# Optimization experiments

Hardware: AMD Instinct MI355X
Metric: run time of the kernel (lower is better)

## Reference

```python
import jax, jax.numpy as jnp
import numpy as np

D_MODEL = 1024
NUM_HEADS = 16
DEPTH = D_MODEL // NUM_HEADS
B, S = 2, 2048


def setup_inputs() -> dict:
    key = jax.random.key(0)
    ks = jax.random.split(key, 11)
    sc = 1.0 / np.sqrt(D_MODEL)
    inp = {
        "q": jax.random.normal(ks[0], (B, S, D_MODEL), jnp.float32),
        "k": jax.random.normal(ks[1], (B, S, D_MODEL), jnp.float32),
        "v": jax.random.normal(ks[2], (B, S, D_MODEL), jnp.float32),
        # 1 = masked (upper triangle), broadcastable to [B,H,S,S]
        "mask": jnp.triu(jnp.ones((S, S), jnp.float32), k=1)[None, None],
        "wq": jax.random.normal(ks[3], (D_MODEL, D_MODEL), jnp.float32) * sc,
        "bq": jnp.zeros((D_MODEL,), jnp.float32),
        "wk": jax.random.normal(ks[4], (D_MODEL, D_MODEL), jnp.float32) * sc,
        "bk": jnp.zeros((D_MODEL,), jnp.float32),
        "wv": jax.random.normal(ks[5], (D_MODEL, D_MODEL), jnp.float32) * sc,
        "bv": jnp.zeros((D_MODEL,), jnp.float32),
        "wo": jax.random.normal(ks[6], (D_MODEL, D_MODEL), jnp.float32) * sc,
        "bo": jnp.zeros((D_MODEL,), jnp.float32),
    }
    return inp


def _split_heads(x):
    b, s, _ = x.shape
    return x.reshape(b, s, NUM_HEADS, DEPTH).transpose(0, 2, 1, 3)  # [B,H,S,D]


def reference(q, k, v, mask, wq, bq, wk, bk, wv, bv, wo, bo):
    qh = _split_heads(q @ wq + bq)
    kh = _split_heads(k @ wk + bk)
    vh = _split_heads(v @ wv + bv)
    logits = jnp.einsum("bhqd,bhkd->bhqk", qh, kh) / jnp.sqrt(
        jnp.asarray(DEPTH, qh.dtype))
    logits = logits + mask * (-1e9)
    attn = jax.nn.softmax(logits, axis=-1)  # [B,H,S,S]
    ctx = jnp.einsum("bhqk,bhkd->bhqd", attn, vh)
    concat = ctx.transpose(0, 2, 1, 3).reshape(q.shape[0], -1, D_MODEL)
    out = concat @ wo + bo
    return out, attn
```

## Files before the change

### kernel.cpp

```cpp
#include <hip/hip_runtime.h>
#include <cstdint>
#include <cstddef>

#define BATCH   2
#define SEQ     2048
#define DMODEL  1024
#define NHEADS  16
#define DHEAD   64
#define TOKENS  (BATCH*SEQ)

typedef __bf16 bf16_t;
typedef bf16_t bf16x8 __attribute__((ext_vector_type(8)));
typedef bf16_t bf16x4 __attribute__((ext_vector_type(4)));
typedef float  f32x4  __attribute__((ext_vector_type(4)));

__device__ __forceinline__ f32x4 mfma16(bf16x8 a, bf16x8 b, f32x4 c) {
    return __builtin_amdgcn_mfma_f32_16x16x32_bf16(a, b, c, 0, 0, 0);
}

__global__ __launch_bounds__(256) void conv_w(
    const float* __restrict__ W, bf16_t* __restrict__ Wt)
{
    __shared__ bf16_t tl[64][65];
    const int t  = threadIdx.x;
    const int kb = blockIdx.y * 64;
    const int nb = blockIdx.x * 64;
    const int r  = t >> 2;
    const int cs = (t & 3) * 16;

    const float* src = W + (size_t)(kb + r)*DMODEL + nb + cs;
    #pragma unroll
    for (int j = 0; j < 4; ++j) {
        float4 u = ((const float4*)src)[j];
        tl[r][cs + j*4 + 0] = (bf16_t)u.x;
        tl[r][cs + j*4 + 1] = (bf16_t)u.y;
        tl[r][cs + j*4 + 2] = (bf16_t)u.z;
        tl[r][cs + j*4 + 3] = (bf16_t)u.w;
    }
    __syncthreads();
    bf16_t* dst = Wt + (size_t)(nb + r)*DMODEL + kb + cs;
    #pragma unroll
    for (int h = 0; h < 2; ++h) {
        bf16x8 o;
        #pragma unroll
        for (int j = 0; j < 8; ++j) o[j] = tl[cs + h*8 + j][r];
        *(bf16x8*)(dst + h*8) = o;
    }
}

template<int IN_BF16, int MODE>
__global__ __launch_bounds__(256, 2) void proj_gemm(
    const void* __restrict__ xin, const bf16_t* __restrict__ Wt,
    const float* __restrict__ bias, void* __restrict__ out)
{
    __shared__ __align__(16) bf16_t Xl[128*72];
    __shared__ __align__(16) bf16_t Wl[64*72];

    const int t    = threadIdx.x;
    const int w    = t >> 6;
    const int lane = t & 63;
    const int quad = lane >> 4;
    const int l16  = lane & 15;
    const int m0   = blockIdx.y * 128;
    const int n0   = blockIdx.x * 64;

    f32x4 acc[2][4] = {};

    for (int kt = 0; kt < DMODEL/64; ++kt) {
        __syncthreads();
        #pragma unroll
        for (int it = 0; it < 4; ++it) {
            int s   = t + it*256;
            int row = s >> 3, seg = s & 7;
            if (IN_BF16) {
                const bf16_t* xb = (const bf16_t*)xin + (size_t)(m0+row)*DMODEL + kt*64 + seg*8;
                *(bf16x8*)&Xl[row*72 + seg*8] = *(const bf16x8*)xb;
            } else {
                const float* xf = (const float*)xin + (size_t)(m0+row)*DMODEL + kt*64 + seg*8;
                float4 u0 = *(const float4*)xf;
                float4 u1 = *(const float4*)(xf + 4);
                bf16x8 vv;
                vv[0]=(bf16_t)u0.x; vv[1]=(bf16_t)u0.y; vv[2]=(bf16_t)u0.z; vv[3]=(bf16_t)u0.w;
                vv[4]=(bf16_t)u1.x; vv[5]=(bf16_t)u1.y; vv[6]=(bf16_t)u1.z; vv[7]=(bf16_t)u1.w;
                *(bf16x8*)&Xl[row*72 + seg*8] = vv;
            }
        }
        #pragma unroll
        for (int it = 0; it < 2; ++it) {
            int s = t + it*256;
            int n = s >> 3, seg = s & 7;
            *(bf16x8*)&Wl[n*72 + seg*8] =
                *(const bf16x8*)(Wt + (size_t)(n0+n)*DMODEL + kt*64 + seg*8);
        }
        __syncthreads();

        #pragma unroll
        for (int kk = 0; kk < 2; ++kk) {
            bf16x8 a0 = *(const bf16x8*)&Xl[(w*32      + l16)*72 + kk*32 + quad*8];
            bf16x8 a1 = *(const bf16x8*)&Xl[(w*32 + 16 + l16)*72 + kk*32 + quad*8];
            #pragma unroll
            for (int c = 0; c < 4; ++c) {
                bf16x8 b = *(const bf16x8*)&Wl[(c*16 + l16)*72 + kk*32 + quad*8];
                acc[0][c] = mfma16(a0, b, acc[0][c]);
                acc[1][c] = mfma16(a1, b, acc[1][c]);
            }
        }
    }

    #pragma unroll
    for (int r = 0; r < 2; ++r) {
        #pragma unroll
        for (int c = 0; c < 4; ++c) {
            int n = n0 + c*16 + l16;
            float bv = bias[n];
            #pragma unroll
            for (int reg = 0; reg < 4; ++reg) {
                int gm = m0 + w*32 + r*16 + quad*4 + reg;
                float val = acc[r][c][reg] + bv;
                if (MODE == 2) {
                    ((float*)out)[(size_t)gm*DMODEL + n] = val;
                } else {
                    int b = gm >> 11, sTok = gm & (SEQ-1);
                    int h = n >> 6,  d    = n & (DHEAD-1);
                    if (MODE == 0)
                        ((bf16_t*)out)[(((size_t)(b*NHEADS + h))*SEQ + sTok)*DHEAD + d] = (bf16_t)val;
                    else
                        ((bf16_t*)out)[(((size_t)(b*NHEADS + h))*DHEAD + d)*SEQ + sTok] = (bf16_t)val;
                }
            }
        }
    }
}

__global__ __launch_bounds__(256, 2) void attn_kernel(
    const bf16_t* __restrict__ Qh, const bf16_t* __restrict__ Kh,
    const bf16_t* __restrict__ Vt, float* __restrict__ attn,
    bf16_t* __restrict__ ctx)
{
    __shared__ __align__(16) bf16_t Ql[64*72];
    __shared__ __align__(16) bf16_t Kl[64*72];
    __shared__ __align__(16) bf16_t Vl[64*72];
    __shared__ __align__(16) bf16_t Pl[4][16*72];

    const int t    = threadIdx.x;
    const int w    = t >> 6;
    const int lane = t & 63;
    const int quad = lane >> 4;
    const int l16  = lane & 15;
    const int bh   = blockIdx.y;
    const int q0   = blockIdx.x * 64;

    const bf16_t* Qp = Qh + (size_t)bh * SEQ * DHEAD;
    const bf16_t* Kp = Kh + (size_t)bh * SEQ * DHEAD;
    const bf16_t* Vp = Vt + (size_t)bh * DHEAD * SEQ;
    float* attp = attn + (size_t)bh * SEQ * SEQ;

    #pragma unroll
    for (int it = 0; it < 2; ++it) {
        int s = t + it*256;
        int row = s >> 3, seg = s & 7;
        *(bf16x8*)&Ql[row*72 + seg*8] =
            *(const bf16x8*)(Qp + (size_t)(q0 + row)*DHEAD + seg*8);
    }
    __syncthreads();
    bf16x8 bq[2];
    bq[0] = *(const bf16x8*)&Ql[(w*16 + l16)*72 +      quad*8];
    bq[1] = *(const bf16x8*)&Ql[(w*16 + l16)*72 + 32 + quad*8];

    const int nkt  = q0/64 + 1;
    const int qrow = q0 + w*16 + l16;
    const float C1 = 0.18033688011112042f;

    float m2 = -1e30f, l2 = 0.f;

    for (int kt = 0; kt < nkt; ++kt) {
        __syncthreads();
        #pragma unroll
        for (int it = 0; it < 2; ++it) {
            int s = t + it*256;
            int row = s >> 3, seg = s & 7;
            *(bf16x8*)&Kl[row*72 + seg*8] =
                *(const bf16x8*)(Kp + (size_t)(kt*64 + row)*DHEAD + seg*8);
        }
        __syncthreads();

        f32x4 sf[4] = {};
        #pragma unroll
        for (int kk = 0; kk < 2; ++kk) {
            #pragma unroll
            for (int c = 0; c < 4; ++c) {
                bf16x8 ak = *(const bf16x8*)&Kl[(c*16 + l16)*72 + kk*32 + quad*8];
                sf[c] = mfma16(ak, bq[kk], sf[c]);
            }
        }
        float tm = -1e30f;
        #pragma unroll
        for (int c = 0; c < 4; ++c) {
            int colb = kt*64 + c*16 + quad*4;
            #pragma unroll
            for (int reg = 0; reg < 4; ++reg) {
                float z = sf[c][reg] * C1;
                z = (colb + reg > qrow) ? -1e30f : z;
                sf[c][reg] = z;
                tm = fmaxf(tm, z);
            }
        }
        tm = fmaxf(tm, __shfl_xor(tm, 16));
        tm = fmaxf(tm, __shfl_xor(tm, 32));
        float mnew = fmaxf(m2, tm);
        float ps = 0.f;
        #pragma unroll
        for (int c = 0; c < 4; ++c)
            #pragma unroll
            for (int reg = 0; reg < 4; ++reg)
                ps += exp2f(sf[c][reg] - mnew);
        ps += __shfl_xor(ps, 16);
        ps += __shfl_xor(ps, 32);
        l2 = l2 * exp2f(m2 - mnew) + ps;
        m2 = mnew;
    }
    const float invl = 1.0f / l2;

    f32x4 cacc[4] = {};
    bf16_t* Plw = &Pl[w][0];

    for (int kt = 0; kt < nkt; ++kt) {
        __syncthreads();
        #pragma unroll
        for (int it = 0; it < 2; ++it) {
            int s = t + it*256;
            int row = s >> 3, seg = s & 7;
            *(bf16x8*)&Kl[row*72 + seg*8] =
                *(const bf16x8*)(Kp + (size_t)(kt*64 + row)*DHEAD + seg*8);
            *(bf16x8*)&Vl[row*72 + seg*8] =
                *(const bf16x8*)(Vp + (size_t)row*SEQ + kt*64 + seg*8);
        }
        __syncthreads();

        f32x4 sf[4] = {};
        #pragma unroll
        for (int kk = 0; kk < 2; ++kk) {
            #pragma unroll
            for (int c = 0; c < 4; ++c) {
                bf16x8 ak = *(const bf16x8*)&Kl[(c*16 + l16)*72 + kk*32 + quad*8];
                sf[c] = mfma16(ak, bq[kk], sf[c]);
            }
        }
        #pragma unroll
        for (int c = 0; c < 4; ++c) {
            int colb = kt*64 + c*16 + quad*4;
            f32x4 pv;
            #pragma unroll
            for (int reg = 0; reg < 4; ++reg) {
                float z = sf[c][reg] * C1;
                float p = (colb + reg > qrow) ? 0.0f : exp2f(z - m2) * invl;
                pv[reg] = p;
            }
            __builtin_nontemporal_store(pv,
                (f32x4*)(attp + (size_t)qrow*SEQ + colb));
            bf16x4 pk;
            pk[0]=(bf16_t)pv[0]; pk[1]=(bf16_t)pv[1];
            pk[2]=(bf16_t)pv[2]; pk[3]=(bf16_t)pv[3];
            *(bf16x4*)&Plw[l16*72 + c*16 + quad*4] = pk;
        }
        #pragma unroll
        for (int kk = 0; kk < 2; ++kk) {
            bf16x8 ap = *(const bf16x8*)&Plw[l16*72 + kk*32 + quad*8];
            #pragma unroll
            for (int c = 0; c < 4; ++c) {
                bf16x8 bv = *(const bf16x8*)&Vl[(c*16 + l16)*72 + kk*32 + quad*8];
                cacc[c] = mfma16(ap, bv, cacc[c]);
            }
        }
    }

    {
        const int r = t >> 2;
        const int c4base = nkt*16 + (t & 3);
        f32x4 z = {0.f, 0.f, 0.f, 0.f};
        float* rowp = attp + (size_t)(q0 + r)*SEQ;
        for (int c4 = c4base; c4 < SEQ/4; c4 += 4)
            __builtin_nontemporal_store(z, (f32x4*)rowp + c4);
    }

    const int b = bh >> 4, h = bh & 15;
    #pragma unroll
    for (int c = 0; c < 4; ++c) {
        #pragma unroll
        for (int reg = 0; reg < 4; ++reg) {
            int gq = q0 + w*16 + quad*4 + reg;
            size_t idx = ((size_t)(b*SEQ + gq))*DMODEL + h*DHEAD + c*16 + l16;
            ctx[idx] = (bf16_t)cacc[c][reg];
        }
    }
}

extern "C" void kernel_launch(void* const* d_in, const int* in_sizes, int n_in,
                              void* d_out, int out_size, void* d_ws, size_t ws_size,
                              hipStream_t stream) {
    const float* q  = (const float*)d_in[0];
    const float* k  = (const float*)d_in[1];
    const float* v  = (const float*)d_in[2];
    const float* wq = (const float*)d_in[4];
    const float* bq = (const float*)d_in[5];
    const float* wk = (const float*)d_in[6];
    const float* bk = (const float*)d_in[7];
    const float* wv = (const float*)d_in[8];
    const float* bv = (const float*)d_in[9];
    const float* wo = (const float*)d_in[10];
    const float* bo = (const float*)d_in[11];

    float* out  = (float*)d_out;
    float* attn = out + (size_t)TOKENS * DMODEL;

    bf16_t* Qws = (bf16_t*)d_ws;
    bf16_t* Kws = Qws + (size_t)TOKENS * DMODEL;
    bf16_t* Vws = Kws + (size_t)TOKENS * DMODEL;
    bf16_t* Cws = Vws + (size_t)TOKENS * DMODEL;

    bf16_t* WtA = (bf16_t*)attn;
    bf16_t* WtB = Qws;

    dim3 blk(256);
    dim3 gconv(DMODEL/64, DMODEL/64);
    dim3 gproj(DMODEL/64, TOKENS/128);

    conv_w<<<gconv, blk, 0, stream>>>(wq, WtA);
    proj_gemm<0,0><<<gproj, blk, 0, stream>>>(q, WtA, bq, Qws);
    conv_w<<<gconv, blk, 0, stream>>>(wk, WtA);
    proj_gemm<0,0><<<gproj, blk, 0, stream>>>(k, WtA, bk, Kws);
    conv_w<<<gconv, blk, 0, stream>>>(wv, WtA);
    proj_gemm<0,1><<<gproj, blk, 0, stream>>>(v, WtA, bv, Vws);

    dim3 gattn(SEQ/64, BATCH*NHEADS);
    attn_kernel<<<gattn, blk, 0, stream>>>(Qws, Kws, Vws, attn, Cws);

    conv_w<<<gconv, blk, 0, stream>>>(wo, WtB);
    proj_gemm<1,2><<<gproj, blk, 0, stream>>>(Cws, WtB, bo, out);
}
```

Measured before the change: 937.9 us.

## Batch weight/input bf16 conversion, skip mask on off-diagonal tiles, reverse attention block order

```diff
diff --git a/kernel.cpp b/kernel.cpp
--- a/kernel.cpp
+++ b/kernel.cpp
@@ -18,7 +18,7 @@
     return __builtin_amdgcn_mfma_f32_16x16x32_bf16(a, b, c, 0, 0, 0);
 }
 
-__global__ __launch_bounds__(256) void conv_w(
+__device__ __forceinline__ void conv_w_body(
     const float* __restrict__ W, bf16_t* __restrict__ Wt)
 {
     __shared__ bf16_t tl[64][65];
@@ -48,9 +48,43 @@
     }
 }
 
-template<int IN_BF16, int MODE>
-__global__ __launch_bounds__(256, 2) void proj_gemm(
-    const void* __restrict__ xin, const bf16_t* __restrict__ Wt,
+__global__ __launch_bounds__(256) void conv_w1(
+    const float* __restrict__ W, bf16_t* __restrict__ Wt)
+{
+    conv_w_body(W, Wt);
+}
+
+__global__ __launch_bounds__(256) void conv_w3(
+    const float* __restrict__ w0, const float* __restrict__ w1,
+    const float* __restrict__ w2, bf16_t* __restrict__ t0,
+    bf16_t* __restrict__ t1, bf16_t* __restrict__ t2)
+{
+    const int z = blockIdx.z;
+    const float* W  = (z == 0) ? w0 : (z == 1) ? w1 : w2;
+    bf16_t*      Wt = (z == 0) ? t0 : (z == 1) ? t1 : t2;
+    conv_w_body(W, Wt);
+}
+
+__global__ __launch_bounds__(256) void conv_x3(
+    const float* __restrict__ x0, const float* __restrict__ x1,
+    const float* __restrict__ x2, bf16_t* __restrict__ y0,
+    bf16_t* __restrict__ y1, bf16_t* __restrict__ y2)
+{
+    const int z = blockIdx.z;
+    const float* xs = (z == 0) ? x0 : (z == 1) ? x1 : x2;
+    bf16_t*      ys = (z == 0) ? y0 : (z == 1) ? y1 : y2;
+    const size_t base = ((size_t)blockIdx.x*256 + threadIdx.x) * 8;
+    float4 u0 = ((const float4*)(xs + base))[0];
+    float4 u1 = ((const float4*)(xs + base))[1];
+    bf16x8 vv;
+    vv[0]=(bf16_t)u0.x; vv[1]=(bf16_t)u0.y; vv[2]=(bf16_t)u0.z; vv[3]=(bf16_t)u0.w;
+    vv[4]=(bf16_t)u1.x; vv[5]=(bf16_t)u1.y; vv[6]=(bf16_t)u1.z; vv[7]=(bf16_t)u1.w;
+    *(bf16x8*)(ys + base) = vv;
+}
+
+template<int MODE>
+__global__ __launch_bounds__(256, 4) void proj_gemm(
+    const bf16_t* __restrict__ xin, const bf16_t* __restrict__ Wt,
     const float* __restrict__ bias, void* __restrict__ out)
 {
     __shared__ __align__(16) bf16_t Xl[128*72];
@@ -72,18 +106,8 @@
         for (int it = 0; it < 4; ++it) {
             int s   = t + it*256;
             int row = s >> 3, seg = s & 7;
-            if (IN_BF16) {
-                const bf16_t* xb = (const bf16_t*)xin + (size_t)(m0+row)*DMODEL + kt*64 + seg*8;
-                *(bf16x8*)&Xl[row*72 + seg*8] = *(const bf16x8*)xb;
-            } else {
-                const float* xf = (const float*)xin + (size_t)(m0+row)*DMODEL + kt*64 + seg*8;
-                float4 u0 = *(const float4*)xf;
-                float4 u1 = *(const float4*)(xf + 4);
-                bf16x8 vv;
-                vv[0]=(bf16_t)u0.x; vv[1]=(bf16_t)u0.y; vv[2]=(bf16_t)u0.z; vv[3]=(bf16_t)u0.w;
-                vv[4]=(bf16_t)u1.x; vv[5]=(bf16_t)u1.y; vv[6]=(bf16_t)u1.z; vv[7]=(bf16_t)u1.w;
-                *(bf16x8*)&Xl[row*72 + seg*8] = vv;
-            }
+            *(bf16x8*)&Xl[row*72 + seg*8] =
+                *(const bf16x8*)(xin + (size_t)(m0+row)*DMODEL + kt*64 + seg*8);
         }
         #pragma unroll
         for (int it = 0; it < 2; ++it) {
@@ -132,7 +156,7 @@
     }
 }
 
-__global__ __launch_bounds__(256, 2) void attn_kernel(
+__global__ __launch_bounds__(256, 4) void attn_kernel(
     const bf16_t* __restrict__ Qh, const bf16_t* __restrict__ Kh,
     const bf16_t* __restrict__ Vt, float* __restrict__ attn,
     bf16_t* __restrict__ ctx)
@@ -148,7 +172,7 @@
     const int quad = lane >> 4;
     const int l16  = lane & 15;
     const int bh   = blockIdx.y;
-    const int q0   = blockIdx.x * 64;
+    const int q0   = (gridDim.x - 1 - blockIdx.x) * 64;
 
     const bf16_t* Qp = Qh + (size_t)bh * SEQ * DHEAD;
     const bf16_t* Kp = Kh + (size_t)bh * SEQ * DHEAD;
@@ -194,16 +218,27 @@
             }
         }
         float tm = -1e30f;
-        #pragma unroll
-        for (int c = 0; c < 4; ++c) {
-            int colb = kt*64 + c*16 + quad*4;
-            #pragma unroll
-            for (int reg = 0; reg < 4; ++reg) {
-                float z = sf[c][reg] * C1;
-                z = (colb + reg > qrow) ? -1e30f : z;
-                sf[c][reg] = z;
-                tm = fmaxf(tm, z);
-            }
+        if (kt == nkt - 1) {
+            #pragma unroll
+            for (int c = 0; c < 4; ++c) {
+                int colb = kt*64 + c*16 + quad*4;
+                #pragma unroll
+                for (int reg = 0; reg < 4; ++reg) {
+                    float z = sf[c][reg] * C1;
+                    z = (colb + reg > qrow) ? -1e30f : z;
+                    sf[c][reg] = z;
+                    tm = fmaxf(tm, z);
+                }
+            }
+        } else {
+            #pragma unroll
+            for (int c = 0; c < 4; ++c)
+                #pragma unroll
+                for (int reg = 0; reg < 4; ++reg) {
+                    float z = sf[c][reg] * C1;
+                    sf[c][reg] = z;
+                    tm = fmaxf(tm, z);
+                }
         }
         tm = fmaxf(tm, __shfl_xor(tm, 16));
         tm = fmaxf(tm, __shfl_xor(tm, 32));
@@ -246,18 +281,23 @@
                 sf[c] = mfma16(ak, bq[kk], sf[c]);
             }
         }
+        const bool diag = (kt == nkt - 1);
         #pragma unroll
         for (int c = 0; c < 4; ++c) {
             int colb = kt*64 + c*16 + quad*4;
             f32x4 pv;
-            #pragma unroll
-            for (int reg = 0; reg < 4; ++reg) {
-                float z = sf[c][reg] * C1;
-                float p = (colb + reg > qrow) ? 0.0f : exp2f(z - m2) * invl;
-                pv[reg] = p;
-            }
-            __builtin_nontemporal_store(pv,
-                (f32x4*)(attp + (size_t)qrow*SEQ + colb));
+            if (diag) {
+                #pragma unroll
+                for (int reg = 0; reg < 4; ++reg) {
+                    float z = sf[c][reg] * C1;
+                    pv[reg] = (colb + reg > qrow) ? 0.0f : exp2f(z - m2) * invl;
+                }
+            } else {
+                #pragma unroll
+                for (int reg = 0; reg < 4; ++reg)
+                    pv[reg] = exp2f(sf[c][reg] * C1 - m2) * invl;
+            }
+            *(f32x4*)(attp + (size_t)qrow*SEQ + colb) = pv;
             bf16x4 pk;
             pk[0]=(bf16_t)pv[0]; pk[1]=(bf16_t)pv[1];
             pk[2]=(bf16_t)pv[2]; pk[3]=(bf16_t)pv[3];
@@ -280,7 +320,7 @@
         f32x4 z = {0.f, 0.f, 0.f, 0.f};
         float* rowp = attp + (size_t)(q0 + r)*SEQ;
         for (int c4 = c4base; c4 < SEQ/4; c4 += 4)
-            __builtin_nontemporal_store(z, (f32x4*)rowp + c4);
+            ((f32x4*)rowp)[c4] = z;
     }
 
     const int b = bh >> 4, h = bh & 15;
@@ -318,23 +358,31 @@
     bf16_t* Vws = Kws + (size_t)TOKENS * DMODEL;
     bf16_t* Cws = Vws + (size_t)TOKENS * DMODEL;
 
-    bf16_t* WtA = (bf16_t*)attn;
-    bf16_t* WtB = Qws;
+    const size_t WSZ = (size_t)DMODEL*DMODEL;
+    const size_t XSZ = (size_t)TOKENS*DMODEL;
+    bf16_t* WtQ = (bf16_t*)attn;
+    bf16_t* WtK = WtQ + WSZ;
+    bf16_t* WtV = WtK + WSZ;
+    bf16_t* Xq  = WtV + WSZ;
+    bf16_t* Xk  = Xq + XSZ;
+    bf16_t* Xv  = Xk + XSZ;
+    bf16_t* WtO = Qws;
 
     dim3 blk(256);
-    dim3 gconv(DMODEL/64, DMODEL/64);
+    dim3 gconvw(DMODEL/64, DMODEL/64, 3);
+    dim3 gconvx(XSZ/8/256, 1, 3);
     dim3 gproj(DMODEL/64, TOKENS/128);
 
-    conv_w<<<gconv, blk, 0, stream>>>(wq, WtA);
-    proj_gemm<0,0><<<gproj, blk, 0, stream>>>(q, WtA, bq, Qws);
-    conv_w<<<gconv, blk, 0, stream>>>(wk, WtA);
-    proj_gemm<0,0><<<gproj, blk, 0, stream>>>(k, WtA, bk, Kws);
-    conv_w<<<gconv, blk, 0, stream>>>(wv, WtA);
-    proj_gemm<0,1><<<gproj, blk, 0, stream>>>(v, WtA, bv, Vws);
+    conv_w3<<<gconvw, blk, 0, stream>>>(wq, wk, wv, WtQ, WtK, WtV);
+    conv_x3<<<gconvx, blk, 0, stream>>>(q, k, v, Xq, Xk, Xv);
+    proj_gemm<0><<<gproj, blk, 0, stream>>>(Xq, WtQ, bq, Qws);
+    proj_gemm<0><<<gproj, blk, 0, stream>>>(Xk, WtK, bk, Kws);
+    proj_gemm<1><<<gproj, blk, 0, stream>>>(Xv, WtV, bv, Vws);
 
     dim3 gattn(SEQ/64, BATCH*NHEADS);
     attn_kernel<<<gattn, blk, 0, stream>>>(Qws, Kws, Vws, attn, Cws);
 
-    conv_w<<<gconv, blk, 0, stream>>>(wo, WtB);
-    proj_gemm<1,2><<<gproj, blk, 0, stream>>>(Cws, WtB, bo, out);
-}
+    dim3 gconvw1(DMODEL/64, DMODEL/64);
+    conv_w1<<<gconvw1, blk, 0, stream>>>(wo, WtO);
+    proj_gemm<2><<<gproj, blk, 0, stream>>>(Cws, WtO, bo, out);
+}
```

After: 900.5 us. 4.0% less time.
